# Optimization experiments

Hardware: AMD Instinct MI355X
Metric: run time of the kernel (lower is better)

Reference implementation:

```python
import jax, jax.numpy as jnp
import numpy as np

S, B, M, F, C = 32, 128, 128, 512, 100


def setup_inputs() -> dict:
    key = jax.random.key(0)
    k = jax.random.split(key, 7)
    x = jax.random.normal(k[0], (B, F), dtype=jnp.float32)
    y = jax.random.randint(k[1], (B,), 0, C, dtype=jnp.int32)
    # Z in {-1, +1}: Bernoulli(0.5) sample mapped via 2*b - 1 (mirrors sample_Z)
    Zb = (jax.random.uniform(k[2], (S, B, M)) < 0.5).astype(jnp.float32)
    Z = 2.0 * Zb - 1.0
    alpha_0 = jax.random.normal(k[3], (M,), dtype=jnp.float32)
    init_c = 2.0 / np.sqrt(F)
    alpha = init_c * jax.random.normal(k[4], (M, F), dtype=jnp.float32)
    alpha = alpha / jnp.linalg.norm(alpha, axis=0, keepdims=True)
    beta_0 = jax.random.normal(k[5], (C,), dtype=jnp.float32)
    init_c2 = 2.0 / np.sqrt(M)
    beta = init_c2 * jax.random.normal(k[6], (C, M), dtype=jnp.float32)
    return {"x": x, "y": y, "Z": Z, "alpha_0": alpha_0, "alpha": alpha,
            "beta_0": beta_0, "beta": beta}


def reference(x, y, Z, alpha_0, alpha, beta_0, beta):
    # linear_eta / eta (compute_linear_eta, compute_eta)
    linear_eta = alpha_0[None, :] + x @ alpha.T            # [B, M]
    eta = jax.nn.sigmoid(linear_eta)                        # exp(l)/(1+exp(l))

    y_onehot = jax.nn.one_hot(y, C, dtype=Z.dtype)          # [B, C]
    # Unperturbed logits shared across all j (rank-1 structure of compute_pi_j)
    base = beta_0[None, None, :] + jnp.einsum('sbm,cm->sbc', Z, beta)  # [S,B,C]

    def pi_for(target):
        # Flipping column j of Z to `target` shifts logits by (target - Z_j)*beta[:, j]
        delta = (target - Z)[..., None] * beta.T[None, None, :, :]  # [S,B,M,C]
        lin = base[:, :, None, :] + delta                            # [S,B,M,C]
        # NOTE: original ADDS the max (faithful to source); softmax ratio unchanged
        lin = lin + jnp.max(lin, axis=-1, keepdims=True)
        num = jnp.sum(y_onehot[None, :, None, :] * lin, axis=-1)     # [S,B,M]
        den = jnp.sum(jnp.exp(lin), axis=-1)                         # [S,B,M]
        return jnp.exp(num) / den                                    # [S,B,M]

    pi_pos = pi_for(1.0)
    pi_neg = pi_for(-1.0)
    # compute_EY_X_j: sum over Monte-Carlo samples
    EY_X_j = jnp.sum(pi_pos * eta[None] + pi_neg * (1.0 - eta)[None], axis=0)  # [B,M]
    return EY_X_j
```

## Files before the change

kernel.cpp:

```cpp
#include <hip/hip_runtime.h>
#include <math.h>

#define S_ 32
#define B_ 128
#define M_ 128
#define F_ 512
#define C_ 100
#define SB 16
#define RWZ 136
#define RWP 136

typedef _Float16 f16;
typedef _Float16 f16x4 __attribute__((ext_vector_type(4)));
typedef _Float16 f16x8 __attribute__((ext_vector_type(8)));
typedef float f32x4 __attribute__((ext_vector_type(4)));

#define WS_BT  0
#define WS_EP  28672
#define WS_EN  61440
#define WS_ETA 94208

__global__ __launch_bounds__(512) void k_pre(
    const float* __restrict__ x, const float* __restrict__ alpha0,
    const float* __restrict__ alpha, const float* __restrict__ beta,
    char* __restrict__ ws, float* __restrict__ out) {
  const int bid = blockIdx.x;
  const int tid = threadIdx.x;
  __shared__ float betaS[C_ * M_];
  if (bid < B_) {
    float* etag = (float*)(ws + WS_ETA);
    const int lane = tid & 63, w = tid >> 6, l15 = lane & 15, lg = lane >> 4;
    if (tid < M_) out[bid * M_ + tid] = 0.f;
    const float4* x4 = (const float4*)x;
    const float4* a4 = (const float4*)alpha;
    float4 xr[8];
#pragma unroll
    for (int r = 0; r < 8; ++r) xr[r] = x4[bid * 128 + r * 16 + l15];
#pragma unroll
    for (int j = 0; j < 4; ++j) {
      int m = w * 16 + j * 4 + lg;
      float acc = 0.f;
#pragma unroll
      for (int r = 0; r < 8; ++r) {
        float4 av = a4[(size_t)m * 128 + r * 16 + l15];
        float4 xv = xr[r];
        acc = fmaf(av.x, xv.x, acc); acc = fmaf(av.y, xv.y, acc);
        acc = fmaf(av.z, xv.z, acc); acc = fmaf(av.w, xv.w, acc);
      }
      acc += __shfl_xor(acc, 1);
      acc += __shfl_xor(acc, 2);
      acc += __shfl_xor(acc, 4);
      acc += __shfl_xor(acc, 8);
      if (l15 == 0) {
        float l = alpha0[m] + acc;
        etag[bid * 128 + m] = 1.f / (1.f + __expf(-l));
      }
    }
  } else {
    for (int i = tid; i < C_ * M_; i += 512) betaS[i] = beta[i];
    __syncthreads();
    const int ci = (bid - B_) * 512 + tid;
    if (ci < 1792) {
      int lane = ci & 63, t = ci >> 6;
      int ct = t % 7, kc = t / 7;
      int c = ct * 16 + (lane & 15);
      int m0 = kc * 32 + (lane >> 4) * 8;
      f16x8 v;
#pragma unroll
      for (int i = 0; i < 8; ++i)
        v[i] = (c < C_) ? (f16)betaS[c * M_ + m0 + i] : (f16)0.f;
      *(f16x8*)(ws + WS_BT + (size_t)ci * 16) = v;
    } else if (ci < 3840) {
      int q = ci - 1792;
      int lane = q & 63, t = q >> 6;
      int m = (t & 7) * 16 + (lane & 15);
      int c0 = (t >> 3) * 32 + (lane >> 4) * 8;
      f16x8 v;
#pragma unroll
      for (int i = 0; i < 8; ++i) {
        int c = c0 + i;
        v[i] = (c < C_) ? (f16)__expf(2.f * betaS[c * M_ + m]) : (f16)0.f;
      }
      *(f16x8*)(ws + WS_EP + (size_t)q * 16) = v;
    } else if (ci < 5888) {
      int q = ci - 3840;
      int lane = q & 63, t = q >> 6;
      int m = (t & 7) * 16 + (lane & 15);
      int c0 = (t >> 3) * 32 + (lane >> 4) * 8;
      f16x8 v;
#pragma unroll
      for (int i = 0; i < 8; ++i) {
        int c = c0 + i;
        v[i] = (c < C_) ? (f16)__expf(-2.f * betaS[c * M_ + m]) : (f16)0.f;
      }
      *(f16x8*)(ws + WS_EN + (size_t)q * 16) = v;
    }
  }
}

__global__ __launch_bounds__(512) void k_main(
    const int* __restrict__ y, const float* __restrict__ Z,
    const float* __restrict__ beta0, const float* __restrict__ beta,
    const char* __restrict__ ws, float* __restrict__ out) {
  const int sh = blockIdx.x;
  const int b = blockIdx.y;
  const int tid = threadIdx.x;
  const int lane = tid & 63;
  const int w = tid >> 6;
  const int l15 = lane & 15;
  const int lg = lane >> 4;

  __shared__ f16 Zf[SB * RWZ];
  __shared__ float baseS[SB * 112];
  __shared__ f16 Pt[SB * RWP];
  __shared__ float PybS[SB];

  const int yb = y[b];
  const int m = w * 16 + l15;

  {
    int p = tid >> 5, q = tid & 31;
    float4 v = ((const float4*)Z)[((size_t)(sh * SB + p) * B_ + b) * 32 + q];
    f16x4 h = {(f16)v.x, (f16)v.y, (f16)v.z, (f16)v.w};
    *(f16x4*)&Zf[p * RWZ + q * 4] = h;
  }

  f16x8 bp[4], bn[4];
#pragma unroll
  for (int kc = 0; kc < 4; ++kc) {
    bp[kc] = *(const f16x8*)(ws + WS_EP + (size_t)((kc * 8 + w) * 64 + lane) * 16);
    bn[kc] = *(const f16x8*)(ws + WS_EN + (size_t)((kc * 8 + w) * 64 + lane) * 16);
  }
  const float bym = beta[yb * M_ + m];
  const float eta_v = ((const float*)(ws + WS_ETA))[b * M_ + m];
  f16x8 bfr[4];
#pragma unroll
  for (int kc = 0; kc < 4; ++kc)
    bfr[kc] = *(const f16x8*)(ws + WS_BT + (size_t)((kc * 7 + (w % 7)) * 64 + lane) * 16);

  __syncthreads();

  if (w < 7) {
    f32x4 acc = {0.f, 0.f, 0.f, 0.f};
    const char* ZfB = (const char*)Zf;
#pragma unroll
    for (int kc = 0; kc < 4; ++kc) {
      f16x8 a0 = *(const f16x8*)(ZfB + l15 * (RWZ * 2) + kc * 64 + lg * 16);
      acc = __builtin_amdgcn_mfma_f32_16x16x32_f16(a0, bfr[kc], acc, 0, 0, 0);
    }
    int col = w * 16 + l15;
    float b0v = (col < C_) ? beta0[col] : 0.f;
#pragma unroll
    for (int j = 0; j < 4; ++j) baseS[(lg * 4 + j) * 112 + col] = acc[j] + b0v;
  }
  __syncthreads();

  {
#pragma unroll
    for (int k = 0; k < 2; ++k) {
      int p = w * 2 + k;
      float v1 = baseS[p * 112 + lane];
      float v2 = (lane < 36) ? baseS[p * 112 + 64 + lane] : -1e30f;
      float mx = fmaxf(v1, v2);
#pragma unroll
      for (int off = 32; off > 0; off >>= 1) mx = fmaxf(mx, __shfl_xor(mx, off));
      float e1 = __expf(v1 - mx);
      float e2 = (lane < 36) ? __expf(v2 - mx) : 0.f;
      float sm = e1 + e2;
#pragma unroll
      for (int off = 32; off > 0; off >>= 1) sm += __shfl_xor(sm, off);
      float rd = 1.f / sm;
      Pt[p * RWP + lane] = (f16)(e1 * rd);
      Pt[p * RWP + 64 + lane] = (f16)((lane < 36) ? e2 * rd : 0.f);
      if (lane == yb) PybS[p] = e1 * rd;
      if (lane + 64 == yb) PybS[p] = e2 * rd;
    }
  }
  __syncthreads();

  {
    f32x4 pA = {0.f, 0.f, 0.f, 0.f}, nA = {0.f, 0.f, 0.f, 0.f};
    const char* PtB = (const char*)Pt;
#pragma unroll
    for (int kc = 0; kc < 4; ++kc) {
      f16x8 a0 = *(const f16x8*)(PtB + l15 * (RWP * 2) + kc * 64 + lg * 16);
      pA = __builtin_amdgcn_mfma_f32_16x16x32_f16(a0, bp[kc], pA, 0, 0, 0);
      nA = __builtin_amdgcn_mfma_f32_16x16x32_f16(a0, bn[kc], nA, 0, 0, 0);
    }
    float epy = __expf(2.f * bym), eny = __expf(-2.f * bym);
    float ome = 1.f - eta_v;
    float o = 0.f;
#pragma unroll
    for (int j = 0; j < 4; ++j) {
      int p = lg * 4 + j;
      float z = (float)Zf[p * RWZ + m];
      float pyb = PybS[p];
      o += (z > 0.f) ? fmaf(pyb, eta_v, (pyb * eny / nA[j]) * ome)
                     : fmaf(pyb * epy / pA[j], eta_v, pyb * ome);
    }
    o += __shfl_xor(o, 16);
    o += __shfl_xor(o, 32);
    if (lane < 16) atomicAdd(&out[b * M_ + w * 16 + l15], o);
  }
}

extern "C" void kernel_launch(void* const* d_in, const int* in_sizes, int n_in,
                              void* d_out, int out_size, void* d_ws, size_t ws_size,
                              hipStream_t stream) {
  const float* x = (const float*)d_in[0];
  const int* y = (const int*)d_in[1];
  const float* Z = (const float*)d_in[2];
  const float* alpha0 = (const float*)d_in[3];
  const float* alpha = (const float*)d_in[4];
  const float* beta0 = (const float*)d_in[5];
  const float* beta = (const float*)d_in[6];
  float* out = (float*)d_out;
  char* ws = (char*)d_ws;

  k_pre<<<dim3(B_ + 12), dim3(512), 0, stream>>>(x, alpha0, alpha, beta, ws, out);
  k_main<<<dim3(2, B_), dim3(512), 0, stream>>>(y, Z, beta0, beta, ws, out);
}
```

Baseline: 14.67 us.

## Fuse pre and main kernels into one cooperative kernel with grid sync

Merges the preprocessing kernel and the main kernel into a single cooperative launch of 256 blocks. A grid-wide barrier replaces the kernel boundary. The beta repacking (transpose and the exp(±2β) tables) is spread across all blocks as scalar f16 scatter writes instead of being done in 12 blocks through a shared-memory staging copy. The Z tile load is also issued before the barrier so it overlaps the prep phase. This removes one launch and the inter-kernel gap, at the cost of grid-sync overhead and uncoalesced 2-byte stores.

```diff
diff --git a/kernel.cpp b/kernel.cpp
--- a/kernel.cpp
+++ b/kernel.cpp
@@ -1,4 +1,5 @@
 #include <hip/hip_runtime.h>
+#include <hip/hip_cooperative_groups.h>
 #include <math.h>
 
 #define S_ 32
@@ -20,22 +21,80 @@
 #define WS_EN  61440
 #define WS_ETA 94208
 
-__global__ __launch_bounds__(512) void k_pre(
-    const float* __restrict__ x, const float* __restrict__ alpha0,
-    const float* __restrict__ alpha, const float* __restrict__ beta,
-    char* __restrict__ ws, float* __restrict__ out) {
-  const int bid = blockIdx.x;
+namespace cg = cooperative_groups;
+
+__global__ __launch_bounds__(512) void k_all(
+    const float* __restrict__ x, const int* __restrict__ y,
+    const float* __restrict__ Z, const float* __restrict__ alpha0,
+    const float* __restrict__ alpha, const float* __restrict__ beta0,
+    const float* __restrict__ beta, char* __restrict__ ws,
+    float* __restrict__ out) {
+  const int gid = blockIdx.x;
+  const int sh = gid >> 7;
+  const int b = gid & 127;
   const int tid = threadIdx.x;
-  __shared__ float betaS[C_ * M_];
-  if (bid < B_) {
+  const int lane = tid & 63;
+  const int w = tid >> 6;
+  const int l15 = lane & 15;
+  const int lg = lane >> 4;
+
+  __shared__ f16 Zf[SB * RWZ];
+  __shared__ float baseS[SB * 112];
+  __shared__ f16 Pt[SB * RWP];
+  __shared__ float PybS[SB];
+
+  {
+    int p = tid >> 5, q = tid & 31;
+    float4 v = ((const float4*)Z)[((size_t)(sh * SB + p) * B_ + b) * 32 + q];
+    f16x4 h = {(f16)v.x, (f16)v.y, (f16)v.z, (f16)v.w};
+    *(f16x4*)&Zf[p * RWZ + q * 4] = h;
+  }
+
+  {
+    const int vid = gid * 512 + tid;
+    if (vid < 12800) {
+      int c = vid >> 7, mm = vid & 127;
+      float bv = beta[vid];
+      {
+        int kc = mm >> 5, lg2 = (mm >> 3) & 3, ii = mm & 7;
+        int ct = c >> 4, cl = c & 15;
+        *(f16*)(ws + WS_BT +
+                (size_t)(((kc * 7 + ct) * 64 + lg2 * 16 + cl) * 16 + ii * 2)) =
+            (f16)bv;
+      }
+      {
+        int mt = mm >> 4, ml = mm & 15;
+        int kc = c >> 5, lg2 = (c >> 3) & 3, ii = c & 7;
+        size_t off = (size_t)(((kc * 8 + mt) * 64 + lg2 * 16 + ml) * 16 + ii * 2);
+        *(f16*)(ws + WS_EP + off) = (f16)__expf(2.f * bv);
+        *(f16*)(ws + WS_EN + off) = (f16)__expf(-2.f * bv);
+      }
+    } else if (vid < 14336) {
+      int rel = vid - 12800;
+      int c = 100 + (rel >> 7), mm = rel & 127;
+      int kc = mm >> 5, lg2 = (mm >> 3) & 3, ii = mm & 7;
+      int ct = c >> 4, cl = c & 15;
+      *(f16*)(ws + WS_BT +
+              (size_t)(((kc * 7 + ct) * 64 + lg2 * 16 + cl) * 16 + ii * 2)) =
+          (f16)0.f;
+    } else if (vid < 17920) {
+      int rel = vid - 14336;
+      int c = 100 + (rel >> 7), mm = rel & 127;
+      int mt = mm >> 4, ml = mm & 15;
+      int kc = c >> 5, lg2 = (c >> 3) & 3, ii = c & 7;
+      size_t off = (size_t)(((kc * 8 + mt) * 64 + lg2 * 16 + ml) * 16 + ii * 2);
+      *(f16*)(ws + WS_EP + off) = (f16)0.f;
+      *(f16*)(ws + WS_EN + off) = (f16)0.f;
+    }
+  }
+
+  if (sh == 0) {
     float* etag = (float*)(ws + WS_ETA);
-    const int lane = tid & 63, w = tid >> 6, l15 = lane & 15, lg = lane >> 4;
-    if (tid < M_) out[bid * M_ + tid] = 0.f;
     const float4* x4 = (const float4*)x;
     const float4* a4 = (const float4*)alpha;
     float4 xr[8];
 #pragma unroll
-    for (int r = 0; r < 8; ++r) xr[r] = x4[bid * 128 + r * 16 + l15];
+    for (int r = 0; r < 8; ++r) xr[r] = x4[b * 128 + r * 16 + l15];
 #pragma unroll
     for (int j = 0; j < 4; ++j) {
       int m = w * 16 + j * 4 + lg;
@@ -53,92 +112,27 @@
       acc += __shfl_xor(acc, 8);
       if (l15 == 0) {
         float l = alpha0[m] + acc;
-        etag[bid * 128 + m] = 1.f / (1.f + __expf(-l));
+        etag[b * 128 + m] = 1.f / (1.f + __expf(-l));
       }
     }
   } else {
-    for (int i = tid; i < C_ * M_; i += 512) betaS[i] = beta[i];
-    __syncthreads();
-    const int ci = (bid - B_) * 512 + tid;
-    if (ci < 1792) {
-      int lane = ci & 63, t = ci >> 6;
-      int ct = t % 7, kc = t / 7;
-      int c = ct * 16 + (lane & 15);
-      int m0 = kc * 32 + (lane >> 4) * 8;
-      f16x8 v;
-#pragma unroll
-      for (int i = 0; i < 8; ++i)
-        v[i] = (c < C_) ? (f16)betaS[c * M_ + m0 + i] : (f16)0.f;
-      *(f16x8*)(ws + WS_BT + (size_t)ci * 16) = v;
-    } else if (ci < 3840) {
-      int q = ci - 1792;
-      int lane = q & 63, t = q >> 6;
-      int m = (t & 7) * 16 + (lane & 15);
-      int c0 = (t >> 3) * 32 + (lane >> 4) * 8;
-      f16x8 v;
-#pragma unroll
-      for (int i = 0; i < 8; ++i) {
-        int c = c0 + i;
-        v[i] = (c < C_) ? (f16)__expf(2.f * betaS[c * M_ + m]) : (f16)0.f;
-      }
-      *(f16x8*)(ws + WS_EP + (size_t)q * 16) = v;
-    } else if (ci < 5888) {
-      int q = ci - 3840;
-      int lane = q & 63, t = q >> 6;
-      int m = (t & 7) * 16 + (lane & 15);
-      int c0 = (t >> 3) * 32 + (lane >> 4) * 8;
-      f16x8 v;
-#pragma unroll
-      for (int i = 0; i < 8; ++i) {
-        int c = c0 + i;
-        v[i] = (c < C_) ? (f16)__expf(-2.f * betaS[c * M_ + m]) : (f16)0.f;
-      }
-      *(f16x8*)(ws + WS_EN + (size_t)q * 16) = v;
-    }
-  }
-}
-
-__global__ __launch_bounds__(512) void k_main(
-    const int* __restrict__ y, const float* __restrict__ Z,
-    const float* __restrict__ beta0, const float* __restrict__ beta,
-    const char* __restrict__ ws, float* __restrict__ out) {
-  const int sh = blockIdx.x;
-  const int b = blockIdx.y;
-  const int tid = threadIdx.x;
-  const int lane = tid & 63;
-  const int w = tid >> 6;
-  const int l15 = lane & 15;
-  const int lg = lane >> 4;
-
-  __shared__ f16 Zf[SB * RWZ];
-  __shared__ float baseS[SB * 112];
-  __shared__ f16 Pt[SB * RWP];
-  __shared__ float PybS[SB];
+    if (tid < M_) out[b * M_ + tid] = 0.f;
+  }
+
+  cg::this_grid().sync();
 
   const int yb = y[b];
   const int m = w * 16 + l15;
 
-  {
-    int p = tid >> 5, q = tid & 31;
-    float4 v = ((const float4*)Z)[((size_t)(sh * SB + p) * B_ + b) * 32 + q];
-    f16x4 h = {(f16)v.x, (f16)v.y, (f16)v.z, (f16)v.w};
-    *(f16x4*)&Zf[p * RWZ + q * 4] = h;
-  }
-
-  f16x8 bp[4], bn[4];
+  f16x8 bp[4], bn[4], bfr[4];
 #pragma unroll
   for (int kc = 0; kc < 4; ++kc) {
     bp[kc] = *(const f16x8*)(ws + WS_EP + (size_t)((kc * 8 + w) * 64 + lane) * 16);
     bn[kc] = *(const f16x8*)(ws + WS_EN + (size_t)((kc * 8 + w) * 64 + lane) * 16);
+    bfr[kc] = *(const f16x8*)(ws + WS_BT + (size_t)((kc * 7 + (w % 7)) * 64 + lane) * 16);
   }
   const float bym = beta[yb * M_ + m];
   const float eta_v = ((const float*)(ws + WS_ETA))[b * M_ + m];
-  f16x8 bfr[4];
-#pragma unroll
-  for (int kc = 0; kc < 4; ++kc)
-    bfr[kc] = *(const f16x8*)(ws + WS_BT + (size_t)((kc * 7 + (w % 7)) * 64 + lane) * 16);
-
-  __syncthreads();
 
   if (w < 7) {
     f32x4 acc = {0.f, 0.f, 0.f, 0.f};
@@ -217,6 +211,9 @@
   float* out = (float*)d_out;
   char* ws = (char*)d_ws;
 
-  k_pre<<<dim3(B_ + 12), dim3(512), 0, stream>>>(x, alpha0, alpha, beta, ws, out);
-  k_main<<<dim3(2, B_), dim3(512), 0, stream>>>(y, Z, beta0, beta, ws, out);
+  void* args[] = {(void*)&x,      (void*)&y,    (void*)&Z,
+                  (void*)&alpha0, (void*)&alpha, (void*)&beta0,
+                  (void*)&beta,   (void*)&ws,   (void*)&out};
+  hipLaunchCooperativeKernel((const void*)k_all, dim3(256), dim3(512), args, 0,
+                             stream);
 }
```

Measured after the change: 54.14 us. 269% more time.

## Halve samples per block, split eta blocks, store MFMA fragments directly in LDS

Applied to the files above, without the earlier changes.

The main kernel now processes 8 samples per block instead of 16, doubling the grid to 4x128 blocks. Z and the softmax probabilities are stored in LDS already arranged as MFMA A-fragments, with the unused rows zero-padded. The eta precompute is split across two blocks per batch row to spread that GEMV over more CUs. The aim is better occupancy and more parallelism for a small latency-bound problem. In exchange, half of each 16-row MFMA tile is wasted and each beta fragment is reloaded by more blocks.

```diff
diff --git a/kernel.cpp b/kernel.cpp
--- a/kernel.cpp
+++ b/kernel.cpp
@@ -6,12 +6,9 @@
 #define M_ 128
 #define F_ 512
 #define C_ 100
-#define SB 16
-#define RWZ 136
-#define RWP 136
+#define SB 8
 
 typedef _Float16 f16;
-typedef _Float16 f16x4 __attribute__((ext_vector_type(4)));
 typedef _Float16 f16x8 __attribute__((ext_vector_type(8)));
 typedef float f32x4 __attribute__((ext_vector_type(4)));
 
@@ -27,18 +24,19 @@
   const int bid = blockIdx.x;
   const int tid = threadIdx.x;
   __shared__ float betaS[C_ * M_];
-  if (bid < B_) {
+  if (bid < 256) {
+    const int b = bid >> 1, mh = bid & 1;
     float* etag = (float*)(ws + WS_ETA);
     const int lane = tid & 63, w = tid >> 6, l15 = lane & 15, lg = lane >> 4;
-    if (tid < M_) out[bid * M_ + tid] = 0.f;
+    if (tid < 64) out[b * M_ + mh * 64 + tid] = 0.f;
     const float4* x4 = (const float4*)x;
     const float4* a4 = (const float4*)alpha;
     float4 xr[8];
 #pragma unroll
-    for (int r = 0; r < 8; ++r) xr[r] = x4[bid * 128 + r * 16 + l15];
-#pragma unroll
-    for (int j = 0; j < 4; ++j) {
-      int m = w * 16 + j * 4 + lg;
+    for (int r = 0; r < 8; ++r) xr[r] = x4[b * 128 + r * 16 + l15];
+#pragma unroll
+    for (int j = 0; j < 2; ++j) {
+      int m = mh * 64 + w * 8 + j * 4 + lg;
       float acc = 0.f;
 #pragma unroll
       for (int r = 0; r < 8; ++r) {
@@ -53,13 +51,13 @@
       acc += __shfl_xor(acc, 8);
       if (l15 == 0) {
         float l = alpha0[m] + acc;
-        etag[bid * 128 + m] = 1.f / (1.f + __expf(-l));
+        etag[b * 128 + m] = 1.f / (1.f + __expf(-l));
       }
     }
   } else {
     for (int i = tid; i < C_ * M_; i += 512) betaS[i] = beta[i];
     __syncthreads();
-    const int ci = (bid - B_) * 512 + tid;
+    const int ci = (bid - 256) * 512 + tid;
     if (ci < 1792) {
       int lane = ci & 63, t = ci >> 6;
       int ct = t % 7, kc = t / 7;
@@ -109,94 +107,109 @@
   const int w = tid >> 6;
   const int l15 = lane & 15;
   const int lg = lane >> 4;
-
-  __shared__ f16 Zf[SB * RWZ];
+  const int s0 = sh * SB;
+
+  __shared__ __align__(16) f16 ZAf[256 * 8];
+  __shared__ __align__(16) f16 PtAf[256 * 8];
   __shared__ float baseS[SB * 112];
-  __shared__ f16 Pt[SB * RWP];
   __shared__ float PybS[SB];
 
   const int yb = y[b];
   const int m = w * 16 + l15;
 
-  {
-    int p = tid >> 5, q = tid & 31;
-    float4 v = ((const float4*)Z)[((size_t)(sh * SB + p) * B_ + b) * 32 + q];
-    f16x4 h = {(f16)v.x, (f16)v.y, (f16)v.z, (f16)v.w};
-    *(f16x4*)&Zf[p * RWZ + q * 4] = h;
-  }
-
-  f16x8 bp[4], bn[4];
+  if (tid < 256) {
+    int s = tid;
+    int kcs = s >> 6, lgs = (s >> 4) & 3, l15s = s & 15;
+    f16x8 hv = {0, 0, 0, 0, 0, 0, 0, 0};
+    if (l15s < SB) {
+      const float* zrow = Z + ((size_t)(s0 + l15s) * B_ + b) * M_ + kcs * 32 + lgs * 8;
+      float4 u0 = *(const float4*)zrow;
+      float4 u1 = *(const float4*)(zrow + 4);
+      hv = (f16x8){(f16)u0.x, (f16)u0.y, (f16)u0.z, (f16)u0.w,
+                   (f16)u1.x, (f16)u1.y, (f16)u1.z, (f16)u1.w};
+    }
+    *(f16x8*)&ZAf[s * 8] = hv;
+  }
+
+  f16x8 bfr[4], bp[4], bn[4];
 #pragma unroll
   for (int kc = 0; kc < 4; ++kc) {
     bp[kc] = *(const f16x8*)(ws + WS_EP + (size_t)((kc * 8 + w) * 64 + lane) * 16);
     bn[kc] = *(const f16x8*)(ws + WS_EN + (size_t)((kc * 8 + w) * 64 + lane) * 16);
+    bfr[kc] = *(const f16x8*)(ws + WS_BT + (size_t)((kc * 7 + (w % 7)) * 64 + lane) * 16);
   }
   const float bym = beta[yb * M_ + m];
   const float eta_v = ((const float*)(ws + WS_ETA))[b * M_ + m];
-  f16x8 bfr[4];
-#pragma unroll
-  for (int kc = 0; kc < 4; ++kc)
-    bfr[kc] = *(const f16x8*)(ws + WS_BT + (size_t)((kc * 7 + (w % 7)) * 64 + lane) * 16);
 
   __syncthreads();
 
   if (w < 7) {
     f32x4 acc = {0.f, 0.f, 0.f, 0.f};
-    const char* ZfB = (const char*)Zf;
 #pragma unroll
     for (int kc = 0; kc < 4; ++kc) {
-      f16x8 a0 = *(const f16x8*)(ZfB + l15 * (RWZ * 2) + kc * 64 + lg * 16);
+      f16x8 a0 = *(const f16x8*)&ZAf[(kc * 64 + lane) * 8];
       acc = __builtin_amdgcn_mfma_f32_16x16x32_f16(a0, bfr[kc], acc, 0, 0, 0);
     }
     int col = w * 16 + l15;
     float b0v = (col < C_) ? beta0[col] : 0.f;
-#pragma unroll
-    for (int j = 0; j < 4; ++j) baseS[(lg * 4 + j) * 112 + col] = acc[j] + b0v;
+    if (lg < 2) {
+#pragma unroll
+      for (int j = 0; j < 4; ++j) baseS[(lg * 4 + j) * 112 + col] = acc[j] + b0v;
+    }
   }
   __syncthreads();
 
   {
-#pragma unroll
-    for (int k = 0; k < 2; ++k) {
-      int p = w * 2 + k;
-      float v1 = baseS[p * 112 + lane];
-      float v2 = (lane < 36) ? baseS[p * 112 + 64 + lane] : -1e30f;
-      float mx = fmaxf(v1, v2);
-#pragma unroll
-      for (int off = 32; off > 0; off >>= 1) mx = fmaxf(mx, __shfl_xor(mx, off));
-      float e1 = __expf(v1 - mx);
-      float e2 = (lane < 36) ? __expf(v2 - mx) : 0.f;
-      float sm = e1 + e2;
-#pragma unroll
-      for (int off = 32; off > 0; off >>= 1) sm += __shfl_xor(sm, off);
-      float rd = 1.f / sm;
-      Pt[p * RWP + lane] = (f16)(e1 * rd);
-      Pt[p * RWP + 64 + lane] = (f16)((lane < 36) ? e2 * rd : 0.f);
-      if (lane == yb) PybS[p] = e1 * rd;
-      if (lane + 64 == yb) PybS[p] = e2 * rd;
-    }
+    int p = w;
+    float v1 = baseS[p * 112 + lane];
+    float v2 = (lane < 36) ? baseS[p * 112 + 64 + lane] : -1e30f;
+    float mx = fmaxf(v1, v2);
+#pragma unroll
+    for (int off = 32; off > 0; off >>= 1) mx = fmaxf(mx, __shfl_xor(mx, off));
+    float e1 = __expf(v1 - mx);
+    float e2 = (lane < 36) ? __expf(v2 - mx) : 0.f;
+    float sm = e1 + e2;
+#pragma unroll
+    for (int off = 32; off > 0; off >>= 1) sm += __shfl_xor(sm, off);
+    float rd = 1.f / sm;
+    float p1 = e1 * rd;
+    float p2 = (lane < 36) ? e2 * rd : 0.f;
+    {
+      int c = lane, kc = c >> 5, lg2 = (c >> 3) & 3, ii = c & 7;
+      PtAf[(kc * 64 + lg2 * 16 + p) * 8 + ii] = (f16)p1;
+      PtAf[(kc * 64 + lg2 * 16 + p + 8) * 8 + ii] = (f16)0.f;
+    }
+    {
+      int c = lane + 64, kc = c >> 5, lg2 = (c >> 3) & 3, ii = c & 7;
+      PtAf[(kc * 64 + lg2 * 16 + p) * 8 + ii] = (f16)p2;
+      PtAf[(kc * 64 + lg2 * 16 + p + 8) * 8 + ii] = (f16)0.f;
+    }
+    if (lane == yb) PybS[p] = p1;
+    if (lane + 64 == yb) PybS[p] = p2;
   }
   __syncthreads();
 
   {
     f32x4 pA = {0.f, 0.f, 0.f, 0.f}, nA = {0.f, 0.f, 0.f, 0.f};
-    const char* PtB = (const char*)Pt;
 #pragma unroll
     for (int kc = 0; kc < 4; ++kc) {
-      f16x8 a0 = *(const f16x8*)(PtB + l15 * (RWP * 2) + kc * 64 + lg * 16);
+      f16x8 a0 = *(const f16x8*)&PtAf[(kc * 64 + lane) * 8];
       pA = __builtin_amdgcn_mfma_f32_16x16x32_f16(a0, bp[kc], pA, 0, 0, 0);
       nA = __builtin_amdgcn_mfma_f32_16x16x32_f16(a0, bn[kc], nA, 0, 0, 0);
     }
-    float epy = __expf(2.f * bym), eny = __expf(-2.f * bym);
+    float epy = __expf(2.f * bym), eny = 1.f / epy;
     float ome = 1.f - eta_v;
     float o = 0.f;
-#pragma unroll
-    for (int j = 0; j < 4; ++j) {
-      int p = lg * 4 + j;
-      float z = (float)Zf[p * RWZ + m];
-      float pyb = PybS[p];
-      o += (z > 0.f) ? fmaf(pyb, eta_v, (pyb * eny / nA[j]) * ome)
-                     : fmaf(pyb * epy / pA[j], eta_v, pyb * ome);
+    int kcz = m >> 5, lgz = (m >> 3) & 3, iiz = m & 7;
+    if (lg < 2) {
+#pragma unroll
+      for (int j = 0; j < 4; ++j) {
+        int p = lg * 4 + j;
+        float z = (float)ZAf[(kcz * 64 + lgz * 16 + p) * 8 + iiz];
+        float pyb = PybS[p];
+        o += (z > 0.f) ? fmaf(pyb, eta_v, (pyb * eny / nA[j]) * ome)
+                       : fmaf(pyb * epy / pA[j], eta_v, pyb * ome);
+      }
     }
     o += __shfl_xor(o, 16);
     o += __shfl_xor(o, 32);
@@ -217,6 +230,6 @@
   float* out = (float*)d_out;
   char* ws = (char*)d_ws;
 
-  k_pre<<<dim3(B_ + 12), dim3(512), 0, stream>>>(x, alpha0, alpha, beta, ws, out);
-  k_main<<<dim3(2, B_), dim3(512), 0, stream>>>(y, Z, beta0, beta, ws, out);
+  k_pre<<<dim3(268), dim3(512), 0, stream>>>(x, alpha0, alpha, beta, ws, out);
+  k_main<<<dim3(4, B_), dim3(512), 0, stream>>>(y, Z, beta0, beta, ws, out);
 }
```

Result: slower. 15.47 us (+5.4%).
